# Kernel optimization log

Measured on AMD Instinct MI355X. Metric: run time of the kernel, lower is better.

## Reference

```python
import jax, jax.numpy as jnp
import numpy as np

N, E, B = 50000, 500000, 2048
IN, ED, H, OUT, P = 64, 16, 64, 64, 1
L, T = 3, 3  # num_layers, num_timesteps
NS = 0.01  # leaky_relu negative slope used throughout AttentiveFP


def _seg_softmax(logits, seg, num):
    # numerically-stable softmax over segments (PyG `softmax`), eps matches PyG
    m = jax.ops.segment_max(logits, seg, num_segments=num)
    e = jnp.exp(logits - m[seg])
    s = jax.ops.segment_sum(e, seg, num_segments=num)
    return e / (s[seg] + 1e-16)


def _gru(xin, h, wx, wh, bx, bh):
    # torch.nn.GRUCell
    gx = xin @ wx.T + bx
    gh = h @ wh.T + bh
    xr, xz, xn = jnp.split(gx, 3, axis=-1)
    hr, hz, hn = jnp.split(gh, 3, axis=-1)
    r = jax.nn.sigmoid(xr + hr)
    z = jax.nn.sigmoid(xz + hz)
    n = jnp.tanh(xn + r * hn)
    return (1.0 - z) * n + z * h


def _forward(x, edge_attr, lin1_w, lin1_b, gate_lin1_w, gate_lin2_w, gate_att_l, gate_att_r, gate_bias,
             gru0_wx, gru0_wh, gru0_bx, gru0_bh,
             atom_lin_w, atom_att_src, atom_att_dst, atom_bias,
             atom_gru_wx, atom_gru_wh, atom_gru_bx, atom_gru_bh,
             mol_lin_w, mol_att_src, mol_att_dst, mol_bias,
             mol_gru_wx, mol_gru_wh, mol_gru_bx, mol_gru_bh,
             lin2_w, lin2_b, ln_g, ln_b, h1_w, h1_b, h2_w, h2_b, h3_w, h3_b,
             edge_index, batch):
    src, dst = edge_index[0], edge_index[1]  # messages flow src -> dst
    x = jax.nn.leaky_relu(x @ lin1_w.T + lin1_b, NS)  # [N, H]
    # --- GATEConv (edge-featured attention) ---
    xj = x[src]  # [E, H]
    e = jax.nn.leaky_relu(jnp.concatenate([xj, edge_attr], axis=-1) @ gate_lin1_w.T, NS)
    alpha = jax.nn.leaky_relu(e @ gate_att_l + x[dst] @ gate_att_r, NS)  # [E]
    alpha = _seg_softmax(alpha, dst, N)
    h = jax.ops.segment_sum((xj @ gate_lin2_w.T) * alpha[:, None], dst, num_segments=N) + gate_bias
    x = jax.nn.relu(_gru(jax.nn.elu(h), x, gru0_wx, gru0_wh, gru0_bx, gru0_bh))
    # --- (num_layers-1) GATConv + GRU layers ---
    for l in range(L - 1):
        xl = x @ atom_lin_w[l].T  # [N, H]
        a = jax.nn.leaky_relu((xl @ atom_att_src[l])[src] + (xl @ atom_att_dst[l])[dst], NS)
        a = _seg_softmax(a, dst, N)
        h = jax.ops.segment_sum(xl[src] * a[:, None], dst, num_segments=N) + atom_bias[l]
        x = jax.nn.relu(_gru(jax.nn.elu(h), x,
                             atom_gru_wx[l], atom_gru_wh[l], atom_gru_bx[l], atom_gru_bh[l]))
    # --- attentive readout over num_timesteps ---
    out = jax.nn.relu(jax.ops.segment_sum(x, batch, num_segments=B))  # [B, H]
    xs = x @ mol_lin_w.T          # bipartite GATConv source transform (fixed)
    a_src = xs @ mol_att_src      # [N]
    for _ in range(T):
        a = jax.nn.leaky_relu(a_src + ((out @ mol_lin_w.T) @ mol_att_dst)[batch], NS)
        a = _seg_softmax(a, batch, B)
        h = jax.nn.elu(jax.ops.segment_sum(xs * a[:, None], batch, num_segments=B) + mol_bias)
        out = jax.nn.relu(_gru(h, out, mol_gru_wx, mol_gru_wh, mol_gru_bx, mol_gru_bh))
    emb = out @ lin2_w.T + lin2_b  # [B, OUT]
    mu = jnp.mean(emb, -1, keepdims=True)
    var = jnp.var(emb, -1, keepdims=True)
    y = (emb - mu) / jnp.sqrt(var + 1e-5) * ln_g + ln_b
    y = jax.nn.relu(y @ h1_w.T + h1_b)
    y = jax.nn.relu(y @ h2_w.T + h2_b)
    return y @ h3_w.T + h3_b  # [B, P]


def setup_inputs() -> dict:
    key = jax.random.key(0)
    ks = iter(jax.random.split(key, 64))
    def w(*s):
        return jax.random.normal(next(ks), s, jnp.float32) * 0.05
    return dict(
        x=jax.random.normal(next(ks), (N, IN), jnp.float32),
        edge_attr=jax.random.normal(next(ks), (E, ED), jnp.float32),
        lin1_w=w(H, IN), lin1_b=w(H),
        gate_lin1_w=w(H, IN + ED), gate_lin2_w=w(H, H),
        gate_att_l=w(H), gate_att_r=w(H), gate_bias=w(H),
        gru0_wx=w(3 * H, H), gru0_wh=w(3 * H, H), gru0_bx=w(3 * H), gru0_bh=w(3 * H),
        atom_lin_w=w(L - 1, H, H), atom_att_src=w(L - 1, H), atom_att_dst=w(L - 1, H), atom_bias=w(L - 1, H),
        atom_gru_wx=w(L - 1, 3 * H, H), atom_gru_wh=w(L - 1, 3 * H, H),
        atom_gru_bx=w(L - 1, 3 * H), atom_gru_bh=w(L - 1, 3 * H),
        mol_lin_w=w(H, H), mol_att_src=w(H), mol_att_dst=w(H), mol_bias=w(H),
        mol_gru_wx=w(3 * H, H), mol_gru_wh=w(3 * H, H), mol_gru_bx=w(3 * H), mol_gru_bh=w(3 * H),
        lin2_w=w(OUT, H), lin2_b=w(OUT),
        ln_g=jnp.ones((OUT,), jnp.float32), ln_b=jnp.zeros((OUT,), jnp.float32),
        h1_w=w(64, OUT), h1_b=w(64), h2_w=w(64, 64), h2_b=w(64), h3_w=w(P, 64), h3_b=w(P),
        edge_index=jax.random.randint(next(ks), (2, E), 0, N, dtype=jnp.int32),
        batch=jnp.sort(jax.random.randint(next(ks), (N,), 0, B, dtype=jnp.int32)),
    )


def reference(x, edge_attr, lin1_w, lin1_b, gate_lin1_w, gate_lin2_w, gate_att_l, gate_att_r, gate_bias, gru0_wx, gru0_wh, gru0_bx, gru0_bh, atom_lin_w, atom_att_src, atom_att_dst, atom_bias, atom_gru_wx, atom_gru_wh, atom_gru_bx, atom_gru_bh, mol_lin_w, mol_att_src, mol_att_dst, mol_bias, mol_gru_wx, mol_gru_wh, mol_gru_bx, mol_gru_bh, lin2_w, lin2_b, ln_g, ln_b, h1_w, h1_b, h2_w, h2_b, h3_w, h3_b, edge_index, batch):
    return _forward(x, edge_attr, lin1_w, lin1_b, gate_lin1_w, gate_lin2_w, gate_att_l, gate_att_r, gate_bias, gru0_wx, gru0_wh, gru0_bx, gru0_bh, atom_lin_w, atom_att_src, atom_att_dst, atom_bias, atom_gru_wx, atom_gru_wh, atom_gru_bx, atom_gru_bh, mol_lin_w, mol_att_src, mol_att_dst, mol_bias, mol_gru_wx, mol_gru_wh, mol_gru_bx, mol_gru_bh, lin2_w, lin2_b, ln_g, ln_b, h1_w, h1_b, h2_w, h2_b, h3_w, h3_b, edge_index, batch)
```

## Files before the change

kernel.cpp:

```cpp
#include <hip/hip_runtime.h>
#include <cfloat>

#define THREADS 256

#define PIN(x) asm volatile("" : "+v"(x))

__device__ __forceinline__ float lrelu01(float v){ return v > 0.f ? v : 0.01f * v; }
__device__ __forceinline__ float reluf(float v){ return v > 0.f ? v : 0.f; }
__device__ __forceinline__ float sigmf(float v){ return 1.f / (1.f + __expf(-v)); }
__device__ __forceinline__ float tanhfast(float v){
    float t = __expf(-2.f * fabsf(v));
    float r = (1.f - t) / (1.f + t);
    return v < 0.f ? -r : r;
}
__device__ __forceinline__ float eluf(float v){ return v > 0.f ? v : __expf(v) - 1.f; }
__device__ __forceinline__ float wmaxf(float v){
    #pragma unroll
    for (int o = 32; o > 0; o >>= 1) v = fmaxf(v, __shfl_xor(v, o, 64));
    return v;
}
__device__ __forceinline__ float wsumf(float v){
    #pragma unroll
    for (int o = 32; o > 0; o >>= 1) v += __shfl_xor(v, o, 64);
    return v;
}

template<int ACT>
__device__ __forceinline__ float actf(float v){
    if (ACT == 1) return lrelu01(v);
    if (ACT == 2) return reluf(v);
    return v;
}

__device__ __forceinline__ void stage_tile(const float* __restrict__ src, float* lds,
                                           int tid, int validf4){
    #pragma unroll
    for (int j = 0; j < 4; ++j){
        int idx = tid + j * 256;
        if (idx < validf4){
            __builtin_amdgcn_global_load_lds(
                (const __attribute__((address_space(1))) void*)(src + (size_t)idx * 4),
                (__attribute__((address_space(3))) void*)(lds + (size_t)idx * 4),
                16, 0, 0);
        }
    }
}

__global__ void k_hist(const int* __restrict__ dst, int* __restrict__ cnt, int E){
    int e = blockIdx.x * blockDim.x + threadIdx.x;
    if (e < E) atomicAdd(&cnt[dst[e]], 1);
}

__global__ void k_scan1(const int* __restrict__ cnt, int* __restrict__ rowptr,
                        int* __restrict__ bsum, int N){
    const int tid = threadIdx.x;
    int i = blockIdx.x * 1024 + tid;
    int v = (i < N) ? cnt[i] : 0;
    int lane = tid & 63, wv = tid >> 6;
    int s = v;
    #pragma unroll
    for (int o = 1; o < 64; o <<= 1){
        int u = __shfl_up(s, o, 64);
        if (lane >= o) s += u;
    }
    __shared__ int wsum[16];
    if (lane == 63) wsum[wv] = s;
    __syncthreads();
    if (wv == 0 && lane < 16){
        int ws = wsum[lane];
        #pragma unroll
        for (int o = 1; o < 16; o <<= 1){
            int u = __shfl_up(ws, o, 64);
            if (lane >= o) ws += u;
        }
        wsum[lane] = ws;
    }
    __syncthreads();
    int woff = wv ? wsum[wv - 1] : 0;
    int incl = s + woff;
    if (i < N) rowptr[i] = incl - v;
    if (tid == 1023) bsum[blockIdx.x] = incl;
}

__global__ void k_scan2(int* __restrict__ bsum, int* __restrict__ rowptr, int NB, int N){
    const int tid = threadIdx.x;
    int v = (tid < NB) ? bsum[tid] : 0;
    int lane = tid & 63, wv = tid >> 6;
    int s = v;
    #pragma unroll
    for (int o = 1; o < 64; o <<= 1){
        int u = __shfl_up(s, o, 64);
        if (lane >= o) s += u;
    }
    __shared__ int wsum[16];
    if (lane == 63) wsum[wv] = s;
    __syncthreads();
    if (wv == 0 && lane < 16){
        int ws = wsum[lane];
        #pragma unroll
        for (int o = 1; o < 16; o <<= 1){
            int u = __shfl_up(ws, o, 64);
            if (lane >= o) ws += u;
        }
        wsum[lane] = ws;
    }
    __syncthreads();
    int woff = wv ? wsum[wv - 1] : 0;
    int incl = s + woff;
    if (tid < NB) bsum[tid] = incl - v;
    if (tid == 1023) rowptr[N] = incl;
}

__global__ void k_scan3(int* __restrict__ rowptr, const int* __restrict__ bsum, int N){
    int i = blockIdx.x * 1024 + threadIdx.x;
    if (i < N) rowptr[i] += bsum[blockIdx.x];
}

__global__ void k_scatter(const int* __restrict__ dst, const int* __restrict__ srcv,
                          const int* __restrict__ rowptr, int* __restrict__ cnt2,
                          int* __restrict__ srcC, int* __restrict__ slot, int E){
    int e = blockIdx.x * blockDim.x + threadIdx.x;
    if (e < E){
        int d = dst[e];
        int p = rowptr[d] + atomicAdd(&cnt2[d], 1);
        srcC[p] = srcv[e];
        slot[e] = p;
    }
}

__global__ void k_browptr(const int* __restrict__ batch, int* __restrict__ rp, int N, int B){
    int n = blockIdx.x * blockDim.x + threadIdx.x;
    if (n >= N) return;
    int b = batch[n];
    int bp = (n == 0) ? -1 : batch[n - 1];
    for (int g = bp + 1; g <= b; ++g) rp[g] = n;
    if (n == N - 1){ for (int g = b + 1; g <= B; ++g) rp[g] = N; }
}

template<int ACT, int NDOT>
__global__ __launch_bounds__(THREADS, 2)
void k_mm64t(const float* __restrict__ in, const float* __restrict__ W, int ldw,
             const float* __restrict__ bias, float* __restrict__ out,
             const float* __restrict__ v0, const float* __restrict__ v1,
             float* __restrict__ o0, float* __restrict__ o1, int rows){
    __shared__ float tile[2][4096];
    const int tid  = threadIdx.x;
    const int lane = tid & 63;
    const int wv   = tid >> 6;
    float w[64];
    #pragma unroll
    for (int k = 0; k < 64; k += 4){
        float4 t4 = *(const float4*)(W + (size_t)lane * ldw + k);
        w[k] = t4.x; w[k+1] = t4.y; w[k+2] = t4.z; w[k+3] = t4.w;
    }
    #pragma unroll
    for (int k = 0; k < 64; ++k) PIN(w[k]);
    const float bb  = bias ? bias[lane] : 0.f;
    const float vl0 = (NDOT > 0) ? v0[lane] : 0.f;
    const float vl1 = (NDOT > 1) ? v1[lane] : 0.f;
    const int ntiles = (rows + 63) >> 6;
    const int totf4  = rows * 16;
    int t = blockIdx.x;
    if (t >= ntiles) return;
    stage_tile(in + (size_t)t * 4096, tile[0], tid, min(1024, totf4 - t * 1024));
    __syncthreads();
    int b = 0;
    while (t < ntiles){
        int tn = t + gridDim.x;
        if (tn < ntiles)
            stage_tile(in + (size_t)tn * 4096, tile[b ^ 1], tid, min(1024, totf4 - tn * 1024));
        #pragma unroll 4
        for (int r = 0; r < 16; ++r){
            int row = wv * 16 + r;
            int g = t * 64 + row;
            const float4* rp = (const float4*)&tile[b][row * 64];
            float a0 = bb, a1 = 0.f, a2 = 0.f, a3 = 0.f;
            #pragma unroll
            for (int kk = 0; kk < 16; ++kk){
                float4 q = rp[kk];
                a0 = fmaf(q.x, w[kk*4],   a0);
                a1 = fmaf(q.y, w[kk*4+1], a1);
                a2 = fmaf(q.z, w[kk*4+2], a2);
                a3 = fmaf(q.w, w[kk*4+3], a3);
            }
            float v = actf<ACT>((a0 + a1) + (a2 + a3));
            if (g < rows){
                out[(size_t)g * 64 + lane] = v;
                if (NDOT > 0){
                    float s0 = wsumf(v * vl0);
                    float s1 = (NDOT > 1) ? wsumf(v * vl1) : 0.f;
                    if (lane == 0){ o0[g] = s0; if (NDOT > 1) o1[g] = s1; }
                }
            }
        }
        __syncthreads();
        b ^= 1; t = tn;
    }
}

__global__ __launch_bounds__(THREADS, 2)
void k_mm64_x2(const float* __restrict__ in,
               const float* __restrict__ W0, int ldw0,
               const float* __restrict__ W1, int ldw1,
               float* __restrict__ out0, float* __restrict__ out1, int rows){
    __shared__ float tile[2][4096];
    const int tid  = threadIdx.x;
    const int lane = tid & 63;
    const int wv   = tid >> 6;
    float w0[64], w1[64];
    #pragma unroll
    for (int k = 0; k < 64; k += 4){
        float4 a = *(const float4*)(W0 + (size_t)lane * ldw0 + k);
        w0[k] = a.x; w0[k+1] = a.y; w0[k+2] = a.z; w0[k+3] = a.w;
        float4 b4 = *(const float4*)(W1 + (size_t)lane * ldw1 + k);
        w1[k] = b4.x; w1[k+1] = b4.y; w1[k+2] = b4.z; w1[k+3] = b4.w;
    }
    #pragma unroll
    for (int k = 0; k < 64; ++k){ PIN(w0[k]); PIN(w1[k]); }
    const int ntiles = (rows + 63) >> 6;
    const int totf4  = rows * 16;
    int t = blockIdx.x;
    if (t >= ntiles) return;
    stage_tile(in + (size_t)t * 4096, tile[0], tid, min(1024, totf4 - t * 1024));
    __syncthreads();
    int b = 0;
    while (t < ntiles){
        int tn = t + gridDim.x;
        if (tn < ntiles)
            stage_tile(in + (size_t)tn * 4096, tile[b ^ 1], tid, min(1024, totf4 - tn * 1024));
        #pragma unroll 2
        for (int r = 0; r < 16; ++r){
            int row = wv * 16 + r;
            int g = t * 64 + row;
            const float4* rp = (const float4*)&tile[b][row * 64];
            float a0 = 0.f, a1 = 0.f, c0 = 0.f, c1 = 0.f;
            #pragma unroll
            for (int kk = 0; kk < 16; ++kk){
                float4 q = rp[kk];
                a0 = fmaf(q.x, w0[kk*4],   a0);
                a1 = fmaf(q.y, w0[kk*4+1], a1);
                a0 = fmaf(q.z, w0[kk*4+2], a0);
                a1 = fmaf(q.w, w0[kk*4+3], a1);
                c0 = fmaf(q.x, w1[kk*4],   c0);
                c1 = fmaf(q.y, w1[kk*4+1], c1);
                c0 = fmaf(q.z, w1[kk*4+2], c0);
                c1 = fmaf(q.w, w1[kk*4+3], c1);
            }
            if (g < rows){
                out0[(size_t)g * 64 + lane] = a0 + a1;
                out1[(size_t)g * 64 + lane] = c0 + c1;
            }
        }
        __syncthreads();
        b ^= 1; t = tn;
    }
}

__global__ __launch_bounds__(THREADS, 2)
void k_gru_wx3(const float* __restrict__ xin, const float* __restrict__ wx,
               const float* __restrict__ bx,
               float* __restrict__ Tr, float* __restrict__ Tz, float* __restrict__ Tn,
               int rows){
    __shared__ float tile[2][4096];
    const int tid  = threadIdx.x;
    const int lane = tid & 63;
    const int wv   = tid >> 6;
    float wr[64], wz[64], wn[64];
    #pragma unroll
    for (int k = 0; k < 64; k += 4){
        float4 a = *(const float4*)(wx + (size_t)lane * 64 + k);
        wr[k] = a.x; wr[k+1] = a.y; wr[k+2] = a.z; wr[k+3] = a.w;
        float4 b4 = *(const float4*)(wx + (size_t)(64 + lane) * 64 + k);
        wz[k] = b4.x; wz[k+1] = b4.y; wz[k+2] = b4.z; wz[k+3] = b4.w;
        float4 c4 = *(const float4*)(wx + (size_t)(128 + lane) * 64 + k);
        wn[k] = c4.x; wn[k+1] = c4.y; wn[k+2] = c4.z; wn[k+3] = c4.w;
    }
    #pragma unroll
    for (int k = 0; k < 64; ++k){ PIN(wr[k]); PIN(wz[k]); PIN(wn[k]); }
    const float br = bx[lane], bz = bx[64 + lane], bn = bx[128 + lane];
    const int ntiles = (rows + 63) >> 6;
    const int totf4  = rows * 16;
    int t = blockIdx.x;
    if (t >= ntiles) return;
    stage_tile(xin + (size_t)t * 4096, tile[0], tid, min(1024, totf4 - t * 1024));
    __syncthreads();
    int b = 0;
    while (t < ntiles){
        int tn = t + gridDim.x;
        if (tn < ntiles)
            stage_tile(xin + (size_t)tn * 4096, tile[b ^ 1], tid, min(1024, totf4 - tn * 1024));
        #pragma unroll 2
        for (int r = 0; r < 16; ++r){
            int row = wv * 16 + r;
            int g = t * 64 + row;
            const float4* rp = (const float4*)&tile[b][row * 64];
            float r0 = br, r1 = 0.f, z0 = bz, z1 = 0.f, n0 = bn, n1 = 0.f;
            #pragma unroll
            for (int kk = 0; kk < 16; ++kk){
                float4 q = rp[kk];
                r0 = fmaf(q.x, wr[kk*4],   r0);
                r1 = fmaf(q.y, wr[kk*4+1], r1);
                r0 = fmaf(q.z, wr[kk*4+2], r0);
                r1 = fmaf(q.w, wr[kk*4+3], r1);
                z0 = fmaf(q.x, wz[kk*4],   z0);
                z1 = fmaf(q.y, wz[kk*4+1], z1);
                z0 = fmaf(q.z, wz[kk*4+2], z0);
                z1 = fmaf(q.w, wz[kk*4+3], z1);
                n0 = fmaf(q.x, wn[kk*4],   n0);
                n1 = fmaf(q.y, wn[kk*4+1], n1);
                n0 = fmaf(q.z, wn[kk*4+2], n0);
                n1 = fmaf(q.w, wn[kk*4+3], n1);
            }
            if (g < rows){
                size_t idx = (size_t)g * 64 + lane;
                Tr[idx] = r0 + r1;
                Tz[idx] = z0 + z1;
                Tn[idx] = n0 + n1;
            }
        }
        __syncthreads();
        b ^= 1; t = tn;
    }
}

__global__ __launch_bounds__(THREADS, 2)
void k_gru_whf(const float* __restrict__ xp, const float* __restrict__ wh,
               const float* __restrict__ bh,
               const float* __restrict__ Tr, const float* __restrict__ Tz,
               const float* __restrict__ Tn, float* __restrict__ out, int rows){
    __shared__ float tile[2][4096];
    const int tid  = threadIdx.x;
    const int lane = tid & 63;
    const int wv   = tid >> 6;
    float wr[64], wz[64], wn[64];
    #pragma unroll
    for (int k = 0; k < 64; k += 4){
        float4 a = *(const float4*)(wh + (size_t)lane * 64 + k);
        wr[k] = a.x; wr[k+1] = a.y; wr[k+2] = a.z; wr[k+3] = a.w;
        float4 b4 = *(const float4*)(wh + (size_t)(64 + lane) * 64 + k);
        wz[k] = b4.x; wz[k+1] = b4.y; wz[k+2] = b4.z; wz[k+3] = b4.w;
        float4 c4 = *(const float4*)(wh + (size_t)(128 + lane) * 64 + k);
        wn[k] = c4.x; wn[k+1] = c4.y; wn[k+2] = c4.z; wn[k+3] = c4.w;
    }
    #pragma unroll
    for (int k = 0; k < 64; ++k){ PIN(wr[k]); PIN(wz[k]); PIN(wn[k]); }
    const float br = bh[lane], bz = bh[64 + lane], bn = bh[128 + lane];
    const int ntiles = (rows + 63) >> 6;
    const int totf4  = rows * 16;
    int t = blockIdx.x;
    if (t >= ntiles) return;
    stage_tile(xp + (size_t)t * 4096, tile[0], tid, min(1024, totf4 - t * 1024));
    __syncthreads();
    int b = 0;
    while (t < ntiles){
        int tn = t + gridDim.x;
        if (tn < ntiles)
            stage_tile(xp + (size_t)tn * 4096, tile[b ^ 1], tid, min(1024, totf4 - tn * 1024));
        #pragma unroll 2
        for (int r = 0; r < 16; ++r){
            int row = wv * 16 + r;
            int g = t * 64 + row;
            const float4* rp = (const float4*)&tile[b][row * 64];
            float r0 = br, r1 = 0.f, z0 = bz, z1 = 0.f, n0 = bn, n1 = 0.f;
            #pragma unroll
            for (int kk = 0; kk < 16; ++kk){
                float4 q = rp[kk];
                r0 = fmaf(q.x, wr[kk*4],   r0);
                r1 = fmaf(q.y, wr[kk*4+1], r1);
                r0 = fmaf(q.z, wr[kk*4+2], r0);
                r1 = fmaf(q.w, wr[kk*4+3], r1);
                z0 = fmaf(q.x, wz[kk*4],   z0);
                z1 = fmaf(q.y, wz[kk*4+1], z1);
                z0 = fmaf(q.z, wz[kk*4+2], z0);
                z1 = fmaf(q.w, wz[kk*4+3], z1);
                n0 = fmaf(q.x, wn[kk*4],   n0);
                n1 = fmaf(q.y, wn[kk*4+1], n1);
                n0 = fmaf(q.z, wn[kk*4+2], n0);
                n1 = fmaf(q.w, wn[kk*4+3], n1);
            }
            if (g < rows){
                size_t idx = (size_t)g * 64 + lane;
                float r_ = sigmf(Tr[idx] + (r0 + r1));
                float z_ = sigmf(Tz[idx] + (z0 + z1));
                float nn = tanhfast(fmaf(r_, n0 + n1, Tn[idx]));
                float xpv = tile[b][row * 64 + lane];
                out[idx] = reluf((1.f - z_) * nn + z_ * xpv);
            }
        }
        __syncthreads();
        b ^= 1; t = tn;
    }
}

__global__ __launch_bounds__(THREADS, 3)
void k_gate_logit(const float* __restrict__ np1, const float* __restrict__ ea,
                  const float* __restrict__ w1,
                  const float* __restrict__ attl, const float* __restrict__ nat,
                  const int* __restrict__ src, const int* __restrict__ dstv,
                  const int* __restrict__ slot, float* __restrict__ logitC, int E){
    __shared__ float wlds[16 * 64];
    __shared__ float al[64];
    for (int i = threadIdx.x; i < 1024; i += blockDim.x){
        int j = i >> 6, k = i & 63;
        wlds[i] = w1[k * 80 + 64 + j];
    }
    if (threadIdx.x < 64) al[threadIdx.x] = attl[threadIdx.x];
    __syncthreads();
    int e = blockIdx.x * blockDim.x + threadIdx.x;
    if (e >= E) return;
    int s = src[e], d = dstv[e];
    float acc[64];
    const float* nr = np1 + (size_t)s * 64;
    #pragma unroll
    for (int k = 0; k < 64; k += 4){
        float4 t = *(const float4*)(nr + k);
        acc[k] = t.x; acc[k+1] = t.y; acc[k+2] = t.z; acc[k+3] = t.w;
    }
    const float* er = ea + (size_t)e * 16;
    #pragma unroll
    for (int j = 0; j < 16; ++j){
        float v = er[j];
        #pragma unroll
        for (int k = 0; k < 64; k += 4){
            float4 t = *(const float4*)&wlds[j * 64 + k];
            acc[k]   = fmaf(v, t.x, acc[k]);
            acc[k+1] = fmaf(v, t.y, acc[k+1]);
            acc[k+2] = fmaf(v, t.z, acc[k+2]);
            acc[k+3] = fmaf(v, t.w, acc[k+3]);
        }
    }
    float l = 0.f;
    #pragma unroll
    for (int k = 0; k < 64; ++k) l = fmaf(lrelu01(acc[k]), al[k], l);
    logitC[slot[e]] = lrelu01(l + nat[d]);
}

__global__ __launch_bounds__(THREADS, 8)
void k_gate_agg(const float* __restrict__ logitC, const int* __restrict__ srcC,
                const int* __restrict__ rowptr,
                const float* __restrict__ xg, const float* __restrict__ bias,
                float* __restrict__ xin, int N){
    const int lane = threadIdx.x & 63;
    const int d = blockIdx.x * (blockDim.x >> 6) + (threadIdx.x >> 6);
    if (d >= N) return;
    int r0 = rowptr[d], r1 = rowptr[d + 1];
    float m = -3.4e38f;
    for (int j = r0 + lane; j < r1; j += 64) m = fmaxf(m, logitC[j]);
    m = wmaxf(m);
    float s0 = 0.f, s1 = 0.f, s2 = 0.f, s3 = 0.f;
    float h0 = 0.f, h1 = 0.f, h2 = 0.f, h3 = 0.f;
    int j = r0;
    for (; j + 3 < r1; j += 4){
        float l0 = logitC[j], l1 = logitC[j+1], l2 = logitC[j+2], l3 = logitC[j+3];
        int n0 = srcC[j], n1 = srcC[j+1], n2 = srcC[j+2], n3 = srcC[j+3];
        float w0 = __expf(l0 - m), w1 = __expf(l1 - m);
        float w2 = __expf(l2 - m), w3 = __expf(l3 - m);
        s0 += w0; s1 += w1; s2 += w2; s3 += w3;
        h0 = fmaf(w0, xg[(size_t)n0 * 64 + lane], h0);
        h1 = fmaf(w1, xg[(size_t)n1 * 64 + lane], h1);
        h2 = fmaf(w2, xg[(size_t)n2 * 64 + lane], h2);
        h3 = fmaf(w3, xg[(size_t)n3 * 64 + lane], h3);
    }
    for (; j < r1; ++j){
        float w0 = __expf(logitC[j] - m);
        s0 += w0;
        h0 = fmaf(w0, xg[(size_t)srcC[j] * 64 + lane], h0);
    }
    float s = (s0 + s1) + (s2 + s3);
    float hk = (h0 + h1) + (h2 + h3);
    float h = hk / (s + 1e-16f) + bias[lane];
    xin[(size_t)d * 64 + lane] = eluf(h);
}

__global__ __launch_bounds__(THREADS, 8)
void k_atom_agg(const float* __restrict__ asrc, const float* __restrict__ adst,
                const int* __restrict__ srcC, const int* __restrict__ rowptr,
                const float* __restrict__ xl,
                const float* __restrict__ bias, float* __restrict__ xin, int N){
    const int lane = threadIdx.x & 63;
    const int d = blockIdx.x * (blockDim.x >> 6) + (threadIdx.x >> 6);
    if (d >= N) return;
    int r0 = rowptr[d], r1 = rowptr[d + 1];
    const float ad = adst[d];
    float m = -3.4e38f;
    for (int j = r0 + lane; j < r1; j += 64)
        m = fmaxf(m, lrelu01(asrc[srcC[j]] + ad));
    m = wmaxf(m);
    float s0 = 0.f, s1 = 0.f, s2 = 0.f, s3 = 0.f;
    float h0 = 0.f, h1 = 0.f, h2 = 0.f, h3 = 0.f;
    int j = r0;
    for (; j + 3 < r1; j += 4){
        int n0 = srcC[j], n1 = srcC[j+1], n2 = srcC[j+2], n3 = srcC[j+3];
        float w0 = __expf(lrelu01(asrc[n0] + ad) - m);
        float w1 = __expf(lrelu01(asrc[n1] + ad) - m);
        float w2 = __expf(lrelu01(asrc[n2] + ad) - m);
        float w3 = __expf(lrelu01(asrc[n3] + ad) - m);
        s0 += w0; s1 += w1; s2 += w2; s3 += w3;
        h0 = fmaf(w0, xl[(size_t)n0 * 64 + lane], h0);
        h1 = fmaf(w1, xl[(size_t)n1 * 64 + lane], h1);
        h2 = fmaf(w2, xl[(size_t)n2 * 64 + lane], h2);
        h3 = fmaf(w3, xl[(size_t)n3 * 64 + lane], h3);
    }
    for (; j < r1; ++j){
        int n0 = srcC[j];
        float w0 = __expf(lrelu01(asrc[n0] + ad) - m);
        s0 += w0;
        h0 = fmaf(w0, xl[(size_t)n0 * 64 + lane], h0);
    }
    float s = (s0 + s1) + (s2 + s3);
    float hk = (h0 + h1) + (h2 + h3);
    float h = hk / (s + 1e-16f) + bias[lane];
    xin[(size_t)d * 64 + lane] = eluf(h);
}

__global__ __launch_bounds__(THREADS, 4)
void k_out0(const float* __restrict__ x, const int* __restrict__ rpB,
            float* __restrict__ outB, int B){
// ... 70 lines not shown
    float y1 = reluf(a1);
    buf1[wv][lane] = y1;
    __syncthreads();
    float a2 = b2[lane];
    #pragma unroll
    for (int k = 0; k < 64; ++k) a2 = fmaf(buf1[wv][k], w2t[k * 64 + lane], a2);
    float y2 = reluf(a2);
    for (int p = 0; p < P; ++p){
        float s = wsumf(y2 * w3[p * 64 + lane]);
        if (lane == 0 && act) out[(size_t)b * P + p] = s + b3[p];
    }
}

extern "C" void kernel_launch(void* const* d_in, const int* in_sizes, int n_in,
                              void* d_out, int out_size, void* d_ws, size_t ws_size,
                              hipStream_t stream){
    const float* x       = (const float*)d_in[0];
    const float* eattr   = (const float*)d_in[1];
    const float* lin1_w  = (const float*)d_in[2];
    const float* lin1_b  = (const float*)d_in[3];
    const float* g_l1w   = (const float*)d_in[4];
    const float* g_l2w   = (const float*)d_in[5];
    const float* g_attl  = (const float*)d_in[6];
    const float* g_attr  = (const float*)d_in[7];
    const float* g_bias  = (const float*)d_in[8];
    const float* gru0_wx = (const float*)d_in[9];
    const float* gru0_wh = (const float*)d_in[10];
    const float* gru0_bx = (const float*)d_in[11];
    const float* gru0_bh = (const float*)d_in[12];
    const float* a_linw  = (const float*)d_in[13];
    const float* a_asrc  = (const float*)d_in[14];
    const float* a_adst  = (const float*)d_in[15];
    const float* a_bias  = (const float*)d_in[16];
    const float* a_gwx   = (const float*)d_in[17];
    const float* a_gwh   = (const float*)d_in[18];
    const float* a_gbx   = (const float*)d_in[19];
    const float* a_gbh   = (const float*)d_in[20];
    const float* m_linw  = (const float*)d_in[21];
    const float* m_asrcv = (const float*)d_in[22];
    const float* m_adstv = (const float*)d_in[23];
    const float* m_bias  = (const float*)d_in[24];
    const float* m_gwx   = (const float*)d_in[25];
    const float* m_gwh   = (const float*)d_in[26];
    const float* m_gbx   = (const float*)d_in[27];
    const float* m_gbh   = (const float*)d_in[28];
    const float* lin2_w  = (const float*)d_in[29];
    const float* lin2_b  = (const float*)d_in[30];
    const float* ln_g    = (const float*)d_in[31];
    const float* ln_b    = (const float*)d_in[32];
    const float* h1_w    = (const float*)d_in[33];
    const float* h1_b    = (const float*)d_in[34];
    const float* h2_w    = (const float*)d_in[35];
    const float* h2_b    = (const float*)d_in[36];
    const float* h3_w    = (const float*)d_in[37];
    const float* h3_b    = (const float*)d_in[38];
    const int*   ei      = (const int*)d_in[39];
    const int*   batch   = (const int*)d_in[40];
    float* out = (float*)d_out;

    const int N = in_sizes[0] / 64;
    const int E = in_sizes[1] / 16;
    const int P = in_sizes[38];
    const int B = out_size / (P > 0 ? P : 1);
    const int* srcv = ei;
    const int* dstv = ei + E;

    float* Wb = (float*)d_ws;
    size_t nb = (size_t)N * 64;
    size_t bb = (size_t)B * 64;
    float* P0 = Wb;
    float* P1 = P0 + nb;
    float* P2 = P1 + nb;
    float* P3 = P2 + nb;
    float* P4 = P3 + nb;
    float* P5 = P4 + nb;
    float* logitC = P5 + nb;
    float* scal  = logitC + E;
    float* outB0 = scal + 2 * (size_t)N;
    float* outB1 = outB0 + bb;
    float* hB    = outB1 + bb;
    float* RB    = hB + bb;
    float* ZB    = RB + bb;
    float* XNB   = ZB + bb;
    int* srcC   = (int*)(XNB + bb);
    int* slot   = srcC + E;
    int* rowptr = slot + E;
    int* cnt    = rowptr + (N + 1);
    int* cnt2   = cnt + N;
    int* rpB    = cnt2 + N;
    int* bsum   = rpB + (B + 1);
    const int NB = (N + 1023) >> 10;
    size_t need = (size_t)((char*)(bsum + NB) - (char*)d_ws);
    if (need > ws_size) return;
    float* embB = XNB;

    dim3 blk(THREADS);
    int gE    = (E + THREADS - 1) / THREADS;
    int gN4   = (N + 3) / 4;
    int gB4   = (B + 3) / 4;
    int gN256 = (N + THREADS - 1) / THREADS;
    int ntN   = (N + 63) >> 6;
    int ntB   = (B + 63) >> 6;
    int GT_N  = ntN < 768 ? ntN : 768;
    int GT_N2 = ntN < 512 ? ntN : 512;
    int GT_B  = ntB;

    hipMemsetAsync(cnt, 0, sizeof(int) * 2 * (size_t)N, stream);
    k_hist<<<gE, blk, 0, stream>>>(dstv, cnt, E);
    k_scan1<<<NB, 1024, 0, stream>>>(cnt, rowptr, bsum, N);
    k_scan2<<<1, 1024, 0, stream>>>(bsum, rowptr, NB, N);
    k_scan3<<<NB, 1024, 0, stream>>>(rowptr, bsum, N);
    k_scatter<<<gE, blk, 0, stream>>>(dstv, srcv, rowptr, cnt2, srcC, slot, E);
    k_browptr<<<gN256, blk, 0, stream>>>(batch, rpB, N, B);

    k_mm64t<1,1><<<GT_N, blk, 0, stream>>>(x, lin1_w, 64, lin1_b, P0,
                                           g_attr, nullptr, scal, nullptr, N);

    k_mm64_x2<<<GT_N2, blk, 0, stream>>>(P0, g_l1w, 80, g_l2w, 64, P1, P2, N);
    k_gate_logit<<<gE, blk, 0, stream>>>(P1, eattr, g_l1w, g_attl, scal, srcv, dstv,
                                         slot, logitC, E);
    k_gate_agg<<<gN4, blk, 0, stream>>>(logitC, srcC, rowptr, P2, g_bias, P3, N);
    k_gru_wx3<<<GT_N2, blk, 0, stream>>>(P3, gru0_wx, gru0_bx, P2, P5, P4, N);
    k_gru_whf<<<GT_N2, blk, 0, stream>>>(P0, gru0_wh, gru0_bh, P2, P5, P4, P1, N);

    k_mm64t<0,2><<<GT_N, blk, 0, stream>>>(P1, a_linw, 64, nullptr, P0,
                                           a_asrc, a_adst, scal, scal + N, N);
    k_atom_agg<<<gN4, blk, 0, stream>>>(scal, scal + N, srcC, rowptr, P0, a_bias, P3, N);
    k_gru_wx3<<<GT_N2, blk, 0, stream>>>(P3, a_gwx, a_gbx, P0, P2, P5, N);
    k_gru_whf<<<GT_N2, blk, 0, stream>>>(P1, a_gwh, a_gbh, P0, P2, P5, P4, N);

    k_mm64t<0,2><<<GT_N, blk, 0, stream>>>(P4, a_linw + 4096, 64, nullptr, P0,
                                           a_asrc + 64, a_adst + 64, scal, scal + N, N);
    k_atom_agg<<<gN4, blk, 0, stream>>>(scal, scal + N, srcC, rowptr, P0, a_bias + 64, P3, N);
    k_gru_wx3<<<GT_N2, blk, 0, stream>>>(P3, a_gwx + 12288, a_gbx + 192, P0, P2, P5, N);
    k_gru_whf<<<GT_N2, blk, 0, stream>>>(P4, a_gwh + 12288, a_gbh + 192, P0, P2, P5, P1, N);

    k_mm64t<0,1><<<GT_N, blk, 0, stream>>>(P1, m_linw, 64, nullptr, P0,
                                           m_asrcv, nullptr, scal, nullptr, N);
    k_out0<<<gB4, blk, 0, stream>>>(P1, rpB, outB0, B);
    float* cur = outB0;
    float* nxt = outB1;
    for (int t = 0; t < 3; ++t){
        k_mol_attn<<<gB4, blk, 0, stream>>>(cur, m_linw, m_adstv, scal, P0, rpB, m_bias, hB, B);
        k_gru_wx3<<<GT_B, blk, 0, stream>>>(hB, m_gwx, m_gbx, RB, ZB, XNB, B);
        k_gru_whf<<<GT_B, blk, 0, stream>>>(cur, m_gwh, m_gbh, RB, ZB, XNB, nxt, B);
        float* tmp = cur; cur = nxt; nxt = tmp;
    }

    k_mm64t<0,0><<<GT_B, blk, 0, stream>>>(cur, lin2_w, 64, lin2_b, embB,
                                           nullptr, nullptr, nullptr, nullptr, B);
    k_head<<<gB4, blk, 0, stream>>>(embB, ln_g, ln_b, h1_w, h1_b, h2_w, h2_b, h3_w, h3_b, out, B, P);
}
```

Baseline: 781.9 us.

## Process gate-logit edges in source-sorted order and hoist GRU loads

Builds a second CSR keyed by source node (extra histogram, scan and scatter) and runs the gate-logit kernel over edges sorted by source, so neighbouring threads gather the same 64-float source rows and cache locality improves. The edge-attribute reads and logit writes become scattered in exchange, and preprocessing gains extra atomics, scans and four E-sized index arrays. It also issues the GRU gate-input loads before the FMA loop so their latency overlaps the compute.

```diff
diff --git a/kernel.cpp b/kernel.cpp
--- a/kernel.cpp
+++ b/kernel.cpp
@@ -46,9 +46,13 @@
     }
 }
 
-__global__ void k_hist(const int* __restrict__ dst, int* __restrict__ cnt, int E){
+__global__ void k_hist2(const int* __restrict__ dst, const int* __restrict__ srcv,
+                        int* __restrict__ cnt, int* __restrict__ cntS, int E){
     int e = blockIdx.x * blockDim.x + threadIdx.x;
-    if (e < E) atomicAdd(&cnt[dst[e]], 1);
+    if (e < E){
+        atomicAdd(&cnt[dst[e]], 1);
+        atomicAdd(&cntS[srcv[e]], 1);
+    }
 }
 
 __global__ void k_scan1(const int* __restrict__ cnt, int* __restrict__ rowptr,
@@ -116,15 +120,19 @@
     if (i < N) rowptr[i] += bsum[blockIdx.x];
 }
 
-__global__ void k_scatter(const int* __restrict__ dst, const int* __restrict__ srcv,
-                          const int* __restrict__ rowptr, int* __restrict__ cnt2,
-                          int* __restrict__ srcC, int* __restrict__ slot, int E){
+__global__ void k_scatter2(const int* __restrict__ dst, const int* __restrict__ srcv,
+                           const int* __restrict__ rowptr, const int* __restrict__ rowptrS,
+                           int* __restrict__ cnt2, int* __restrict__ cntS2,
+                           int* __restrict__ srcC, int* __restrict__ eidS,
+                           int* __restrict__ srcS, int* __restrict__ dstS,
+                           int* __restrict__ slotS, int E){
     int e = blockIdx.x * blockDim.x + threadIdx.x;
     if (e < E){
-        int d = dst[e];
+        int d = dst[e], s = srcv[e];
         int p = rowptr[d] + atomicAdd(&cnt2[d], 1);
-        srcC[p] = srcv[e];
-        slot[e] = p;
+        srcC[p] = s;
+        int q = rowptrS[s] + atomicAdd(&cntS2[s], 1);
+        eidS[q] = e; srcS[q] = s; dstS[q] = d; slotS[q] = p;
     }
 }
 
@@ -360,6 +368,11 @@
         for (int r = 0; r < 16; ++r){
             int row = wv * 16 + r;
             int g = t * 64 + row;
+            bool ok = g < rows;
+            size_t idx = (size_t)g * 64 + lane;
+            float trv = 0.f, tzv = 0.f, tnv = 0.f;
+            if (ok){ trv = Tr[idx]; tzv = Tz[idx]; tnv = Tn[idx]; }
+            float xpv = tile[b][row * 64 + lane];
             const float4* rp = (const float4*)&tile[b][row * 64];
             float r0 = br, r1 = 0.f, z0 = bz, z1 = 0.f, n0 = bn, n1 = 0.f;
             #pragma unroll
@@ -378,12 +391,10 @@
                 n0 = fmaf(q.z, wn[kk*4+2], n0);
                 n1 = fmaf(q.w, wn[kk*4+3], n1);
             }
-            if (g < rows){
-                size_t idx = (size_t)g * 64 + lane;
-                float r_ = sigmf(Tr[idx] + (r0 + r1));
-                float z_ = sigmf(Tz[idx] + (z0 + z1));
-                float nn = tanhfast(fmaf(r_, n0 + n1, Tn[idx]));
-                float xpv = tile[b][row * 64 + lane];
+            if (ok){
+                float r_ = sigmf(trv + (r0 + r1));
+                float z_ = sigmf(tzv + (z0 + z1));
+                float nn = tanhfast(fmaf(r_, n0 + n1, tnv));
                 out[idx] = reluf((1.f - z_) * nn + z_ * xpv);
             }
         }
@@ -393,11 +404,12 @@
 }
 
 __global__ __launch_bounds__(THREADS, 3)
-void k_gate_logit(const float* __restrict__ np1, const float* __restrict__ ea,
-                  const float* __restrict__ w1,
-                  const float* __restrict__ attl, const float* __restrict__ nat,
-                  const int* __restrict__ src, const int* __restrict__ dstv,
-                  const int* __restrict__ slot, float* __restrict__ logitC, int E){
+void k_gate_logit_s(const float* __restrict__ np1, const float* __restrict__ ea,
+                    const float* __restrict__ w1,
+                    const float* __restrict__ attl, const float* __restrict__ nat,
+                    const int* __restrict__ eidS, const int* __restrict__ srcS,
+                    const int* __restrict__ dstS, const int* __restrict__ slotS,
+                    float* __restrict__ logitC, int E){
     __shared__ float wlds[16 * 64];
     __shared__ float al[64];
     for (int i = threadIdx.x; i < 1024; i += blockDim.x){
@@ -406,9 +418,9 @@
     }
     if (threadIdx.x < 64) al[threadIdx.x] = attl[threadIdx.x];
     __syncthreads();
-    int e = blockIdx.x * blockDim.x + threadIdx.x;
-    if (e >= E) return;
-    int s = src[e], d = dstv[e];
+    int j = blockIdx.x * blockDim.x + threadIdx.x;
+    if (j >= E) return;
+    int s = srcS[j], e = eidS[j], d = dstS[j];
     float acc[64];
     const float* nr = np1 + (size_t)s * 64;
     #pragma unroll
@@ -418,11 +430,11 @@
     }
     const float* er = ea + (size_t)e * 16;
     #pragma unroll
-    for (int j = 0; j < 16; ++j){
-        float v = er[j];
+    for (int jj = 0; jj < 16; ++jj){
+        float v = er[jj];
         #pragma unroll
         for (int k = 0; k < 64; k += 4){
-            float4 t = *(const float4*)&wlds[j * 64 + k];
+            float4 t = *(const float4*)&wlds[jj * 64 + k];
             acc[k]   = fmaf(v, t.x, acc[k]);
             acc[k+1] = fmaf(v, t.y, acc[k+1]);
             acc[k+2] = fmaf(v, t.z, acc[k+2]);
@@ -432,7 +444,7 @@
     float l = 0.f;
     #pragma unroll
     for (int k = 0; k < 64; ++k) l = fmaf(lrelu01(acc[k]), al[k], l);
-    logitC[slot[e]] = lrelu01(l + nat[d]);
+    logitC[slotS[j]] = lrelu01(l + nat[d]);
 }
 
 __global__ __launch_bounds__(THREADS, 8)
@@ -669,16 +681,22 @@
     float* RB    = hB + bb;
     float* ZB    = RB + bb;
     float* XNB   = ZB + bb;
-    int* srcC   = (int*)(XNB + bb);
-    int* slot   = srcC + E;
-    int* rowptr = slot + E;
-    int* cnt    = rowptr + (N + 1);
-    int* cnt2   = cnt + N;
-    int* rpB    = cnt2 + N;
-    int* bsum   = rpB + (B + 1);
+    int* srcC    = (int*)(XNB + bb);
+    int* eidS    = srcC + E;
+    int* srcS    = eidS + E;
+    int* dstS    = srcS + E;
+    int* slotS   = dstS + E;
+    int* rowptr  = slotS + E;
+    int* rowptrS = rowptr + (N + 1);
+    int* cnt     = rowptrS + (N + 1);
+    int* rpB     = cnt + 4 * (size_t)N;
+    int* bsum    = rpB + (B + 1);
     const int NB = (N + 1023) >> 10;
     size_t need = (size_t)((char*)(bsum + NB) - (char*)d_ws);
     if (need > ws_size) return;
+    int* cnt2  = cnt + N;
+    int* cntS  = cnt + 2 * (size_t)N;
+    int* cntS2 = cnt + 3 * (size_t)N;
     float* embB = XNB;
 
     dim3 blk(THREADS);
@@ -692,20 +710,24 @@
     int GT_N2 = ntN < 512 ? ntN : 512;
     int GT_B  = ntB;
 
-    hipMemsetAsync(cnt, 0, sizeof(int) * 2 * (size_t)N, stream);
-    k_hist<<<gE, blk, 0, stream>>>(dstv, cnt, E);
+    hipMemsetAsync(cnt, 0, sizeof(int) * 4 * (size_t)N, stream);
+    k_hist2<<<gE, blk, 0, stream>>>(dstv, srcv, cnt, cntS, E);
     k_scan1<<<NB, 1024, 0, stream>>>(cnt, rowptr, bsum, N);
     k_scan2<<<1, 1024, 0, stream>>>(bsum, rowptr, NB, N);
     k_scan3<<<NB, 1024, 0, stream>>>(rowptr, bsum, N);
-    k_scatter<<<gE, blk, 0, stream>>>(dstv, srcv, rowptr, cnt2, srcC, slot, E);
+    k_scan1<<<NB, 1024, 0, stream>>>(cntS, rowptrS, bsum, N);
+    k_scan2<<<1, 1024, 0, stream>>>(bsum, rowptrS, NB, N);
+    k_scan3<<<NB, 1024, 0, stream>>>(rowptrS, bsum, N);
+    k_scatter2<<<gE, blk, 0, stream>>>(dstv, srcv, rowptr, rowptrS, cnt2, cntS2,
+                                       srcC, eidS, srcS, dstS, slotS, E);
     k_browptr<<<gN256, blk, 0, stream>>>(batch, rpB, N, B);
 
     k_mm64t<1,1><<<GT_N, blk, 0, stream>>>(x, lin1_w, 64, lin1_b, P0,
                                            g_attr, nullptr, scal, nullptr, N);
 
     k_mm64_x2<<<GT_N2, blk, 0, stream>>>(P0, g_l1w, 80, g_l2w, 64, P1, P2, N);
-    k_gate_logit<<<gE, blk, 0, stream>>>(P1, eattr, g_l1w, g_attl, scal, srcv, dstv,
-                                         slot, logitC, E);
+    k_gate_logit_s<<<gE, blk, 0, stream>>>(P1, eattr, g_l1w, g_attl, scal,
+                                           eidS, srcS, dstS, slotS, logitC, E);
     k_gate_agg<<<gN4, blk, 0, stream>>>(logitC, srcC, rowptr, P2, g_bias, P3, N);
     k_gru_wx3<<<GT_N2, blk, 0, stream>>>(P3, gru0_wx, gru0_bx, P2, P5, P4, N);
     k_gru_whf<<<GT_N2, blk, 0, stream>>>(P0, gru0_wh, gru0_bh, P2, P5, P4, P1, N);
```

Result: slower. 828.7 us (+6.0%).

## Split GRU gate kernels into narrower passes to cut register pressure

Applied to the files above, without the earlier changes.

Each pair of GRU kernels, which held 192 weight registers per thread, becomes four passes: an r/z input projection, an n-gate input projection through the existing mm64t kernel, a hidden-side r/z pass that writes sigmoids in place, and a final n-gate pass. With fewer pinned weights per thread, launch bounds go from 2 to 3 blocks per CU and the grid grows, which should raise occupancy. The cost is more launches and extra global traffic, since the inputs are re-read and the R/Z/XN intermediates make additional round trips.

```diff
diff --git a/kernel.cpp b/kernel.cpp
--- a/kernel.cpp
+++ b/kernel.cpp
@@ -256,28 +256,25 @@
     }
 }
 
-__global__ __launch_bounds__(THREADS, 2)
-void k_gru_wx3(const float* __restrict__ xin, const float* __restrict__ wx,
+__global__ __launch_bounds__(THREADS, 3)
+void k_gru_rz2(const float* __restrict__ xin, const float* __restrict__ wx,
                const float* __restrict__ bx,
-               float* __restrict__ Tr, float* __restrict__ Tz, float* __restrict__ Tn,
-               int rows){
+               float* __restrict__ Tr, float* __restrict__ Tz, int rows){
     __shared__ float tile[2][4096];
     const int tid  = threadIdx.x;
     const int lane = tid & 63;
     const int wv   = tid >> 6;
-    float wr[64], wz[64], wn[64];
+    float wr[64], wz[64];
     #pragma unroll
     for (int k = 0; k < 64; k += 4){
         float4 a = *(const float4*)(wx + (size_t)lane * 64 + k);
         wr[k] = a.x; wr[k+1] = a.y; wr[k+2] = a.z; wr[k+3] = a.w;
         float4 b4 = *(const float4*)(wx + (size_t)(64 + lane) * 64 + k);
         wz[k] = b4.x; wz[k+1] = b4.y; wz[k+2] = b4.z; wz[k+3] = b4.w;
-        float4 c4 = *(const float4*)(wx + (size_t)(128 + lane) * 64 + k);
-        wn[k] = c4.x; wn[k+1] = c4.y; wn[k+2] = c4.z; wn[k+3] = c4.w;
-    }
-    #pragma unroll
-    for (int k = 0; k < 64; ++k){ PIN(wr[k]); PIN(wz[k]); PIN(wn[k]); }
-    const float br = bx[lane], bz = bx[64 + lane], bn = bx[128 + lane];
+    }
+    #pragma unroll
+    for (int k = 0; k < 64; ++k){ PIN(wr[k]); PIN(wz[k]); }
+    const float br = bx[lane], bz = bx[64 + lane];
     const int ntiles = (rows + 63) >> 6;
     const int totf4  = rows * 16;
     int t = blockIdx.x;
@@ -294,7 +291,7 @@
             int row = wv * 16 + r;
             int g = t * 64 + row;
             const float4* rp = (const float4*)&tile[b][row * 64];
-            float r0 = br, r1 = 0.f, z0 = bz, z1 = 0.f, n0 = bn, n1 = 0.f;
+            float r0 = br, r1 = 0.f, z0 = bz, z1 = 0.f;
             #pragma unroll
             for (int kk = 0; kk < 16; ++kk){
                 float4 q = rp[kk];
@@ -306,16 +303,11 @@
                 z1 = fmaf(q.y, wz[kk*4+1], z1);
                 z0 = fmaf(q.z, wz[kk*4+2], z0);
                 z1 = fmaf(q.w, wz[kk*4+3], z1);
-                n0 = fmaf(q.x, wn[kk*4],   n0);
-                n1 = fmaf(q.y, wn[kk*4+1], n1);
-                n0 = fmaf(q.z, wn[kk*4+2], n0);
-                n1 = fmaf(q.w, wn[kk*4+3], n1);
             }
             if (g < rows){
                 size_t idx = (size_t)g * 64 + lane;
                 Tr[idx] = r0 + r1;
                 Tz[idx] = z0 + z1;
-                Tn[idx] = n0 + n1;
             }
         }
         __syncthreads();
@@ -323,28 +315,25 @@
     }
 }
 
-__global__ __launch_bounds__(THREADS, 2)
-void k_gru_whf(const float* __restrict__ xp, const float* __restrict__ wh,
-               const float* __restrict__ bh,
-               const float* __restrict__ Tr, const float* __restrict__ Tz,
-               const float* __restrict__ Tn, float* __restrict__ out, int rows){
+__global__ __launch_bounds__(THREADS, 3)
+void k_gru_sig2(const float* __restrict__ xp, const float* __restrict__ wh,
+                const float* __restrict__ bh,
+                float* __restrict__ Tr, float* __restrict__ Tz, int rows){
     __shared__ float tile[2][4096];
     const int tid  = threadIdx.x;
     const int lane = tid & 63;
     const int wv   = tid >> 6;
-    float wr[64], wz[64], wn[64];
+    float wr[64], wz[64];
     #pragma unroll
     for (int k = 0; k < 64; k += 4){
         float4 a = *(const float4*)(wh + (size_t)lane * 64 + k);
         wr[k] = a.x; wr[k+1] = a.y; wr[k+2] = a.z; wr[k+3] = a.w;
         float4 b4 = *(const float4*)(wh + (size_t)(64 + lane) * 64 + k);
         wz[k] = b4.x; wz[k+1] = b4.y; wz[k+2] = b4.z; wz[k+3] = b4.w;
-        float4 c4 = *(const float4*)(wh + (size_t)(128 + lane) * 64 + k);
-        wn[k] = c4.x; wn[k+1] = c4.y; wn[k+2] = c4.z; wn[k+3] = c4.w;
-    }
-    #pragma unroll
-    for (int k = 0; k < 64; ++k){ PIN(wr[k]); PIN(wz[k]); PIN(wn[k]); }
-    const float br = bh[lane], bz = bh[64 + lane], bn = bh[128 + lane];
+    }
+    #pragma unroll
+    for (int k = 0; k < 64; ++k){ PIN(wr[k]); PIN(wz[k]); }
+    const float br = bh[lane], bz = bh[64 + lane];
     const int ntiles = (rows + 63) >> 6;
     const int totf4  = rows * 16;
     int t = blockIdx.x;
@@ -360,8 +349,12 @@
         for (int r = 0; r < 16; ++r){
             int row = wv * 16 + r;
             int g = t * 64 + row;
+            bool ok = g < rows;
+            size_t idx = (size_t)g * 64 + lane;
+            float trv = 0.f, tzv = 0.f;
+            if (ok){ trv = Tr[idx]; tzv = Tz[idx]; }
             const float4* rp = (const float4*)&tile[b][row * 64];
-            float r0 = br, r1 = 0.f, z0 = bz, z1 = 0.f, n0 = bn, n1 = 0.f;
+            float r0 = br, r1 = 0.f, z0 = bz, z1 = 0.f;
             #pragma unroll
             for (int kk = 0; kk < 16; ++kk){
                 float4 q = rp[kk];
@@ -373,18 +366,69 @@
                 z1 = fmaf(q.y, wz[kk*4+1], z1);
                 z0 = fmaf(q.z, wz[kk*4+2], z0);
                 z1 = fmaf(q.w, wz[kk*4+3], z1);
-                n0 = fmaf(q.x, wn[kk*4],   n0);
-                n1 = fmaf(q.y, wn[kk*4+1], n1);
-                n0 = fmaf(q.z, wn[kk*4+2], n0);
-                n1 = fmaf(q.w, wn[kk*4+3], n1);
-            }
-            if (g < rows){
-                size_t idx = (size_t)g * 64 + lane;
-                float r_ = sigmf(Tr[idx] + (r0 + r1));
-                float z_ = sigmf(Tz[idx] + (z0 + z1));
-                float nn = tanhfast(fmaf(r_, n0 + n1, Tn[idx]));
-                float xpv = tile[b][row * 64 + lane];
-                out[idx] = reluf((1.f - z_) * nn + z_ * xpv);
+            }
+            if (ok){
+                Tr[idx] = sigmf(trv + (r0 + r1));
+                Tz[idx] = sigmf(tzv + (z0 + z1));
+            }
+        }
+        __syncthreads();
+        b ^= 1; t = tn;
+    }
+}
+
+__global__ __launch_bounds__(THREADS, 3)
+void k_gru_fin3_t(const float* __restrict__ xp, const float* __restrict__ whn,
+                  const float* __restrict__ bhn,
+                  const float* __restrict__ XN, const float* __restrict__ R,
+                  const float* __restrict__ Z, float* __restrict__ out, int rows){
+    __shared__ float tile[2][4096];
+    const int tid  = threadIdx.x;
+    const int lane = tid & 63;
+    const int wv   = tid >> 6;
+    float w[64];
+    #pragma unroll
+    for (int k = 0; k < 64; k += 4){
+        float4 t4 = *(const float4*)(whn + (size_t)lane * 64 + k);
+        w[k] = t4.x; w[k+1] = t4.y; w[k+2] = t4.z; w[k+3] = t4.w;
+    }
+    #pragma unroll
+    for (int k = 0; k < 64; ++k) PIN(w[k]);
+    const float bb = bhn[lane];
+    const int ntiles = (rows + 63) >> 6;
+    const int totf4  = rows * 16;
+    int t = blockIdx.x;
+    if (t >= ntiles) return;
+    stage_tile(xp + (size_t)t * 4096, tile[0], tid, min(1024, totf4 - t * 1024));
+    __syncthreads();
+    int b = 0;
+    while (t < ntiles){
+        int tn = t + gridDim.x;
+        if (tn < ntiles)
+            stage_tile(xp + (size_t)tn * 4096, tile[b ^ 1], tid, min(1024, totf4 - tn * 1024));
+        #pragma unroll 4
+        for (int r = 0; r < 16; ++r){
+            int row = wv * 16 + r;
+            int g = t * 64 + row;
+            bool ok = g < rows;
+            size_t idx = (size_t)g * 64 + lane;
+            float rr = 0.f, zz = 0.f, xn = 0.f;
+            if (ok){ rr = R[idx]; zz = Z[idx]; xn = XN[idx]; }
+            const float4* rp = (const float4*)&tile[b][row * 64];
+            float a0 = bb, a1 = 0.f, a2 = 0.f, a3 = 0.f;
+            #pragma unroll
+            for (int kk = 0; kk < 16; ++kk){
+                float4 q = rp[kk];
+                a0 = fmaf(q.x, w[kk*4],   a0);
+                a1 = fmaf(q.y, w[kk*4+1], a1);
+                a2 = fmaf(q.z, w[kk*4+2], a2);
+                a3 = fmaf(q.w, w[kk*4+3], a3);
+            }
+            if (ok){
+                float hn = (a0 + a1) + (a2 + a3);
+                float hp = tile[b][row * 64 + lane];
+                float nn = tanhfast(fmaf(rr, hn, xn));
+                out[idx] = reluf((1.f - zz) * nn + zz * hp);
             }
         }
         __syncthreads();
@@ -689,7 +733,7 @@
     int ntN   = (N + 63) >> 6;
     int ntB   = (B + 63) >> 6;
     int GT_N  = ntN < 768 ? ntN : 768;
-    int GT_N2 = ntN < 512 ? ntN : 512;
+    int GT_N3 = ntN < 768 ? ntN : 768;
     int GT_B  = ntB;
 
     hipMemsetAsync(cnt, 0, sizeof(int) * 2 * (size_t)N, stream);
@@ -703,24 +747,36 @@
     k_mm64t<1,1><<<GT_N, blk, 0, stream>>>(x, lin1_w, 64, lin1_b, P0,
                                            g_attr, nullptr, scal, nullptr, N);
 
-    k_mm64_x2<<<GT_N2, blk, 0, stream>>>(P0, g_l1w, 80, g_l2w, 64, P1, P2, N);
+    k_mm64_x2<<<GT_N, blk, 0, stream>>>(P0, g_l1w, 80, g_l2w, 64, P1, P2, N);
     k_gate_logit<<<gE, blk, 0, stream>>>(P1, eattr, g_l1w, g_attl, scal, srcv, dstv,
                                          slot, logitC, E);
     k_gate_agg<<<gN4, blk, 0, stream>>>(logitC, srcC, rowptr, P2, g_bias, P3, N);
-    k_gru_wx3<<<GT_N2, blk, 0, stream>>>(P3, gru0_wx, gru0_bx, P2, P5, P4, N);
-    k_gru_whf<<<GT_N2, blk, 0, stream>>>(P0, gru0_wh, gru0_bh, P2, P5, P4, P1, N);
+    k_gru_rz2<<<GT_N3, blk, 0, stream>>>(P3, gru0_wx, gru0_bx, P2, P5, N);
+    k_mm64t<0,0><<<GT_N, blk, 0, stream>>>(P3, gru0_wx + 8192, 64, gru0_bx + 128, P4,
+                                           nullptr, nullptr, nullptr, nullptr, N);
+    k_gru_sig2<<<GT_N3, blk, 0, stream>>>(P0, gru0_wh, gru0_bh, P2, P5, N);
+    k_gru_fin3_t<<<GT_N3, blk, 0, stream>>>(P0, gru0_wh + 8192, gru0_bh + 128,
+                                            P4, P2, P5, P1, N);
 
     k_mm64t<0,2><<<GT_N, blk, 0, stream>>>(P1, a_linw, 64, nullptr, P0,
                                            a_asrc, a_adst, scal, scal + N, N);
     k_atom_agg<<<gN4, blk, 0, stream>>>(scal, scal + N, srcC, rowptr, P0, a_bias, P3, N);
-    k_gru_wx3<<<GT_N2, blk, 0, stream>>>(P3, a_gwx, a_gbx, P0, P2, P5, N);
-    k_gru_whf<<<GT_N2, blk, 0, stream>>>(P1, a_gwh, a_gbh, P0, P2, P5, P4, N);
+    k_gru_rz2<<<GT_N3, blk, 0, stream>>>(P3, a_gwx, a_gbx, P0, P2, N);
+    k_mm64t<0,0><<<GT_N, blk, 0, stream>>>(P3, a_gwx + 8192, 64, a_gbx + 128, P5,
+                                           nullptr, nullptr, nullptr, nullptr, N);
+    k_gru_sig2<<<GT_N3, blk, 0, stream>>>(P1, a_gwh, a_gbh, P0, P2, N);
+    k_gru_fin3_t<<<GT_N3, blk, 0, stream>>>(P1, a_gwh + 8192, a_gbh + 128,
+                                            P5, P0, P2, P4, N);
 
     k_mm64t<0,2><<<GT_N, blk, 0, stream>>>(P4, a_linw + 4096, 64, nullptr, P0,
                                            a_asrc + 64, a_adst + 64, scal, scal + N, N);
     k_atom_agg<<<gN4, blk, 0, stream>>>(scal, scal + N, srcC, rowptr, P0, a_bias + 64, P3, N);
-    k_gru_wx3<<<GT_N2, blk, 0, stream>>>(P3, a_gwx + 12288, a_gbx + 192, P0, P2, P5, N);
-    k_gru_whf<<<GT_N2, blk, 0, stream>>>(P4, a_gwh + 12288, a_gbh + 192, P0, P2, P5, P1, N);
+    k_gru_rz2<<<GT_N3, blk, 0, stream>>>(P3, a_gwx + 12288, a_gbx + 192, P0, P2, N);
+    k_mm64t<0,0><<<GT_N, blk, 0, stream>>>(P3, a_gwx + 12288 + 8192, 64, a_gbx + 192 + 128, P5,
+                                           nullptr, nullptr, nullptr, nullptr, N);
+    k_gru_sig2<<<GT_N3, blk, 0, stream>>>(P4, a_gwh + 12288, a_gbh + 192, P0, P2, N);
+    k_gru_fin3_t<<<GT_N3, blk, 0, stream>>>(P4, a_gwh + 12288 + 8192, a_gbh + 192 + 128,
+                                            P5, P0, P2, P1, N);
 
     k_mm64t<0,1><<<GT_N, blk, 0, stream>>>(P1, m_linw, 64, nullptr, P0,
                                            m_asrcv, nullptr, scal, nullptr, N);
@@ -729,8 +785,12 @@
     float* nxt = outB1;
     for (int t = 0; t < 3; ++t){
         k_mol_attn<<<gB4, blk, 0, stream>>>(cur, m_linw, m_adstv, scal, P0, rpB, m_bias, hB, B);
-        k_gru_wx3<<<GT_B, blk, 0, stream>>>(hB, m_gwx, m_gbx, RB, ZB, XNB, B);
-        k_gru_whf<<<GT_B, blk, 0, stream>>>(cur, m_gwh, m_gbh, RB, ZB, XNB, nxt, B);
+        k_gru_rz2<<<GT_B, blk, 0, stream>>>(hB, m_gwx, m_gbx, RB, ZB, B);
+        k_mm64t<0,0><<<GT_B, blk, 0, stream>>>(hB, m_gwx + 8192, 64, m_gbx + 128, XNB,
+                                               nullptr, nullptr, nullptr, nullptr, B);
+        k_gru_sig2<<<GT_B, blk, 0, stream>>>(cur, m_gwh, m_gbh, RB, ZB, B);
+        k_gru_fin3_t<<<GT_B, blk, 0, stream>>>(cur, m_gwh + 8192, m_gbh + 128,
+                                               XNB, RB, ZB, nxt, B);
         float* tmp = cur; cur = nxt; nxt = tmp;
     }
 
```

Result: slower. 958.1 us (+22.5%).

## Rewrite gate logit kernel as wave-per-edge with lane-per-feature and shuffles

Applied to the files above, without the earlier changes.

The GATE edge-logit kernel changes from one thread per edge, which holds 64 accumulators and does uncoalesced per-thread row loads, to one 64-lane wavefront per edge in a grid-stride loop. Each lane keeps its column of edge weights in registers, broadcasts the edge attributes with shuffles and reduces the logit with a wave sum. This is meant to coalesce the gathered node-row reads and ease register pressure, at the cost of a shuffle reduction per edge. Separately, the GRU Wh kernel now issues its Tr/Tz/Tn global loads before the FMA loop so their latency overlaps the compute.

```diff
diff --git a/kernel.cpp b/kernel.cpp
--- a/kernel.cpp
+++ b/kernel.cpp
@@ -360,6 +360,11 @@
         for (int r = 0; r < 16; ++r){
             int row = wv * 16 + r;
             int g = t * 64 + row;
+            bool ok = g < rows;
+            size_t idx = (size_t)g * 64 + lane;
+            float trv = 0.f, tzv = 0.f, tnv = 0.f;
+            if (ok){ trv = Tr[idx]; tzv = Tz[idx]; tnv = Tn[idx]; }
+            float xpv = tile[b][row * 64 + lane];
             const float4* rp = (const float4*)&tile[b][row * 64];
             float r0 = br, r1 = 0.f, z0 = bz, z1 = 0.f, n0 = bn, n1 = 0.f;
             #pragma unroll
@@ -378,12 +383,10 @@
                 n0 = fmaf(q.z, wn[kk*4+2], n0);
                 n1 = fmaf(q.w, wn[kk*4+3], n1);
             }
-            if (g < rows){
-                size_t idx = (size_t)g * 64 + lane;
-                float r_ = sigmf(Tr[idx] + (r0 + r1));
-                float z_ = sigmf(Tz[idx] + (z0 + z1));
-                float nn = tanhfast(fmaf(r_, n0 + n1, Tn[idx]));
-                float xpv = tile[b][row * 64 + lane];
+            if (ok){
+                float r_ = sigmf(trv + (r0 + r1));
+                float z_ = sigmf(tzv + (z0 + z1));
+                float nn = tanhfast(fmaf(r_, n0 + n1, tnv));
                 out[idx] = reluf((1.f - z_) * nn + z_ * xpv);
             }
         }
@@ -392,47 +395,31 @@
     }
 }
 
-__global__ __launch_bounds__(THREADS, 3)
-void k_gate_logit(const float* __restrict__ np1, const float* __restrict__ ea,
-                  const float* __restrict__ w1,
-                  const float* __restrict__ attl, const float* __restrict__ nat,
-                  const int* __restrict__ src, const int* __restrict__ dstv,
-                  const int* __restrict__ slot, float* __restrict__ logitC, int E){
-    __shared__ float wlds[16 * 64];
-    __shared__ float al[64];
-    for (int i = threadIdx.x; i < 1024; i += blockDim.x){
-        int j = i >> 6, k = i & 63;
-        wlds[i] = w1[k * 80 + 64 + j];
-    }
-    if (threadIdx.x < 64) al[threadIdx.x] = attl[threadIdx.x];
-    __syncthreads();
-    int e = blockIdx.x * blockDim.x + threadIdx.x;
-    if (e >= E) return;
-    int s = src[e], d = dstv[e];
-    float acc[64];
-    const float* nr = np1 + (size_t)s * 64;
-    #pragma unroll
-    for (int k = 0; k < 64; k += 4){
-        float4 t = *(const float4*)(nr + k);
-        acc[k] = t.x; acc[k+1] = t.y; acc[k+2] = t.z; acc[k+3] = t.w;
-    }
-    const float* er = ea + (size_t)e * 16;
-    #pragma unroll
-    for (int j = 0; j < 16; ++j){
-        float v = er[j];
+__global__ __launch_bounds__(THREADS, 8)
+void k_gate_logit_w(const float* __restrict__ np1, const float* __restrict__ ea,
+                    const float* __restrict__ w1,
+                    const float* __restrict__ attl, const float* __restrict__ nat,
+                    const int* __restrict__ src, const int* __restrict__ dstv,
+                    const int* __restrict__ slot, float* __restrict__ logitC, int E){
+    const int lane = threadIdx.x & 63;
+    int wid = blockIdx.x * (blockDim.x >> 6) + (threadIdx.x >> 6);
+    int nw  = gridDim.x * (blockDim.x >> 6);
+    float w1e[16];
+    #pragma unroll
+    for (int j = 0; j < 16; ++j) w1e[j] = w1[(size_t)lane * 80 + 64 + j];
+    const float al = attl[lane];
+    for (int e = wid; e < E; e += nw){
+        int s = src[e], d = dstv[e];
+        float acc = np1[(size_t)s * 64 + lane];
+        float eav = ea[(size_t)e * 16 + (lane & 15)];
         #pragma unroll
-        for (int k = 0; k < 64; k += 4){
-            float4 t = *(const float4*)&wlds[j * 64 + k];
-            acc[k]   = fmaf(v, t.x, acc[k]);
-            acc[k+1] = fmaf(v, t.y, acc[k+1]);
-            acc[k+2] = fmaf(v, t.z, acc[k+2]);
-            acc[k+3] = fmaf(v, t.w, acc[k+3]);
+        for (int j = 0; j < 16; ++j){
+            float ej = __shfl(eav, j, 64);
+            acc = fmaf(ej, w1e[j], acc);
         }
-    }
-    float l = 0.f;
-    #pragma unroll
-    for (int k = 0; k < 64; ++k) l = fmaf(lrelu01(acc[k]), al[k], l);
-    logitC[slot[e]] = lrelu01(l + nat[d]);
+        float l = wsumf(lrelu01(acc) * al);
+        if (lane == 0) logitC[slot[e]] = lrelu01(l + nat[d]);
+    }
 }
 
 __global__ __launch_bounds__(THREADS, 8)
@@ -691,6 +678,7 @@
     int GT_N  = ntN < 768 ? ntN : 768;
     int GT_N2 = ntN < 512 ? ntN : 512;
     int GT_B  = ntB;
+    int GL    = 2048;
 
     hipMemsetAsync(cnt, 0, sizeof(int) * 2 * (size_t)N, stream);
     k_hist<<<gE, blk, 0, stream>>>(dstv, cnt, E);
@@ -704,8 +692,8 @@
                                            g_attr, nullptr, scal, nullptr, N);
 
     k_mm64_x2<<<GT_N2, blk, 0, stream>>>(P0, g_l1w, 80, g_l2w, 64, P1, P2, N);
-    k_gate_logit<<<gE, blk, 0, stream>>>(P1, eattr, g_l1w, g_attl, scal, srcv, dstv,
-                                         slot, logitC, E);
+    k_gate_logit_w<<<GL, blk, 0, stream>>>(P1, eattr, g_l1w, g_attl, scal, srcv, dstv,
+                                           slot, logitC, E);
     k_gate_agg<<<gN4, blk, 0, stream>>>(logitC, srcC, rowptr, P2, g_bias, P3, N);
     k_gru_wx3<<<GT_N2, blk, 0, stream>>>(P3, gru0_wx, gru0_bx, P2, P5, P4, N);
     k_gru_whf<<<GT_N2, blk, 0, stream>>>(P0, gru0_wh, gru0_bh, P2, P5, P4, P1, N);
```

Result: slower. 873.7 us (+11.7%).
